# Kernel optimization log

Hardware: AMD Instinct MI355X
Metric: run time of the kernel (lower is better)

The kernel has to match this reference:

```python
import jax, jax.numpy as jnp
import numpy as np

KK = 10.0  # sigmoid sharpness constant `kk` from the source

def sigmoid_k(x):
    return jax.nn.sigmoid(KK * x)

def setup_inputs() -> dict:
    key = jax.random.key(0)
    k1, k2, k3 = jax.random.split(key, 3)
    B, L = 8192, 4096
    # contiguous valid-prefix padding mask with random per-row lengths in [L//4, L)
    lens = jax.random.randint(k1, (B,), L // 4, L)
    mask = (jnp.arange(L)[None, :] < lens[:, None]).astype(jnp.float32)
    t = jax.random.uniform(k2, (B, 1), dtype=jnp.float32) * L          # crop centers
    l = 1.0 + jax.random.uniform(k3, (B, 1), dtype=jnp.float32) * (L / 2.0)  # half-widths
    return {"t": t, "l": l, "mask": mask, "length": L}

def reference(t, l, mask, length):
    t = t.reshape(-1, 1)
    l = l.reshape(-1, 1)
    # boundaries of the valid region (replaces the CPU numpy argmax round-trip)
    left = (jnp.argmax(mask, axis=-1).astype(jnp.float32) - 1.0)[:, None]          # [B,1]
    right = (float(length) - jnp.argmax(mask[:, ::-1], axis=-1).astype(jnp.float32))[:, None]  # [B,1]
    sentence_length = jnp.sum(mask, axis=-1, keepdims=True) / 2.0                   # [B,1]
    l_eff = jnp.where(l <= sentence_length, sentence_length, l)
    t_left = (t - l_eff) * (t - l_eff >= left).astype(jnp.float32)
    t_left = jnp.where(t_left == 0.0, left, t_left)
    t_right = ((t + l_eff) <= right).astype(jnp.float32) * (t + l_eff)
    t_right = jnp.where(t_right == 0.0, right, t_right)
    pos = jnp.arange(length, dtype=jnp.float32)                                     # [L]
    crop_mask = sigmoid_k(pos - t_left) - sigmoid_k(pos - t_right)                  # [B,L]
    crop_mask = (crop_mask >= 0.5).astype(jnp.float32) * mask
    return crop_mask
```

## Files before the change

### kernel.cpp

```cpp
#include <hip/hip_runtime.h>
#include <hip/hip_bf16.h>
#include <climits>


#define BLOCK 256

typedef float nfloat4 __attribute__((ext_vector_type(4)));

__device__ __forceinline__ float sigmoid10(float x) {
    return 1.0f / (1.0f + expf(-10.0f * x));
}
__device__ __forceinline__ float fdiff(float p, float tl, float tr) {
    return sigmoid10(p - tl) - sigmoid10(p - tr);
}

__global__ __launch_bounds__(BLOCK) void probe_kernel(
    const float* __restrict__ t, const float* __restrict__ l,
    const float* __restrict__ mask, int2* __restrict__ ws, int B, int Llen) {
    const int row = blockIdx.x * BLOCK + threadIdx.x;
    if (row >= B) return;
    const float* mrow = mask + (size_t)row * Llen;

    int blo = -1, bhi = Llen;
    #pragma unroll 1
    for (int it = 0; it < 13; ++it) {
        int mid = (blo + bhi) >> 1;
        mid = max(mid, 0);
        const float v = mrow[mid];
        if (v > 0.5f) blo = mid; else bhi = mid;
    }
    const int len = bhi;

    int lo = 1, hi = 0;
    if (len > 0) {
        const float leftf  = -1.0f;
        const float rightf = (float)len;
        const float sl = 0.5f * (float)len;
        const float tv = t[row], lv = l[row];
        const float leff = (lv <= sl) ? sl : lv;
        float tl0 = tv - leff;
        float t_left = (tl0 >= leftf) ? tl0 : 0.0f;
        if (t_left == 0.0f) t_left = leftf;
        float tr0 = tv + leff;
        float t_right = (tr0 <= rightf) ? tr0 : 0.0f;
        if (t_right == 0.0f) t_right = rightf;

        const float c = expf(-10.0f * (t_right - t_left));
        const float b = 1.0f - 3.0f * c;
        const float disc = b * b - 4.0f * c;
        if (b > 0.0f && disc >= 0.0f) {
            const float xp = 0.5f * (b + sqrtf(disc));
            const float p_lo = t_left - 0.1f * logf(xp);
            const float p_hi = (t_left + t_right) - p_lo;
            lo = (int)ceilf(p_lo);
            hi = (int)floorf(p_hi);
            #pragma unroll 1
            for (int k = 0; k < 4 && fdiff((float)(lo - 1), t_left, t_right) >= 0.5f; ++k) --lo;
            #pragma unroll 1
            for (int k = 0; k < 4 && fdiff((float)lo, t_left, t_right) < 0.5f; ++k) ++lo;
            #pragma unroll 1
            for (int k = 0; k < 4 && fdiff((float)(hi + 1), t_left, t_right) >= 0.5f; ++k) ++hi;
            #pragma unroll 1
            for (int k = 0; k < 4 && fdiff((float)hi, t_left, t_right) < 0.5f; ++k) --hi;
        }
        lo = max(lo, 0);
        hi = min(hi, len - 1);
    }
    ws[row] = make_int2(lo, hi);
}

__global__ __launch_bounds__(BLOCK) void ones_kernel(
    const int2* __restrict__ ws, nfloat4* __restrict__ out,
    int nv, int B, int total_waves) {
    const int lane = threadIdx.x & 63;
    const int wave0 = blockIdx.x * (BLOCK / 64) + (threadIdx.x >> 6);

    for (int row = wave0; row < B; row += total_waves) {
        const int2 bnd = ws[row];
        const int lo = bnd.x, hi = bnd.y;
        if (lo > hi) continue;
        const int qA = lo >> 2, qB = hi >> 2;
        nfloat4* orow = out + (size_t)row * nv;
        for (int q = qA + lane; q <= qB; q += 64) {
            const int e = q << 2;
            nfloat4 o;
            o.x = (e     >= lo && e     <= hi) ? 1.0f : 0.0f;
            o.y = (e + 1 >= lo && e + 1 <= hi) ? 1.0f : 0.0f;
            o.z = (e + 2 >= lo && e + 2 <= hi) ? 1.0f : 0.0f;
            o.w = (e + 3 >= lo && e + 3 <= hi) ? 1.0f : 0.0f;
            __builtin_nontemporal_store(o, &orow[q]);
        }
    }
}

extern "C" void kernel_launch(void* const* d_in, const int* in_sizes, int n_in,
                              void* d_out, int out_size, void* d_ws, size_t ws_size,
                              hipStream_t stream) {
    const float* t    = (const float*)d_in[0];
    const float* l    = (const float*)d_in[1];
    const float* mask = (const float*)d_in[2];
    float* out = (float*)d_out;
    int2* ws = (int2*)d_ws;

    const int B = in_sizes[0];
    const int Llen = in_sizes[2] / B;

    hipMemsetAsync(d_out, 0, (size_t)out_size * sizeof(float), stream);

    probe_kernel<<<(B + BLOCK - 1) / BLOCK, BLOCK, 0, stream>>>(t, l, mask, ws, B, Llen);

    const int nv = Llen >> 2;
    const int blocks = 2048;
    const int total_waves = blocks * (BLOCK / 64);
    ones_kernel<<<blocks, BLOCK, 0, stream>>>(ws, (nfloat4*)out, nv, B, total_waves);
}
```

Measured before the change: 224.3 us.

## Drop memset and write full output rows with streaming stores

Removes the separate memset of the output and has the emit kernel write every element of each row, zeros included, so the output is written once instead of memset followed by partial overwrite. Each block handles 32 rows, loading their bounds into shared memory, and stores use inline global_store_dwordx4 with sc0 sc1 nt cache bits. The cost is that each row is written in full by one kernel, plus inline asm that depends on the target ISA.

```diff
diff --git a/kernel.cpp b/kernel.cpp
--- a/kernel.cpp
+++ b/kernel.cpp
@@ -4,8 +4,14 @@
 
 
 #define BLOCK 256
+#define ROWS_PER_BLOCK 32
 
 typedef float nfloat4 __attribute__((ext_vector_type(4)));
+
+__device__ __forceinline__ void store_stream(nfloat4 v, nfloat4* p) {
+    asm volatile("global_store_dwordx4 %0, %1, off sc0 sc1 nt"
+                 :: "v"(p), "v"(v) : "memory");
+}
 
 __device__ __forceinline__ float sigmoid10(float x) {
     return 1.0f / (1.0f + expf(-10.0f * x));
@@ -69,26 +75,42 @@
     ws[row] = make_int2(lo, hi);
 }
 
-__global__ __launch_bounds__(BLOCK) void ones_kernel(
-    const int2* __restrict__ ws, nfloat4* __restrict__ out,
-    int nv, int B, int total_waves) {
-    const int lane = threadIdx.x & 63;
-    const int wave0 = blockIdx.x * (BLOCK / 64) + (threadIdx.x >> 6);
+__global__ __launch_bounds__(BLOCK) void emit_kernel(
+    const int2* __restrict__ ws, nfloat4* __restrict__ out, int nv, int B) {
+    const int tid = threadIdx.x;
+    const int row0 = blockIdx.x * ROWS_PER_BLOCK;
 
-    for (int row = wave0; row < B; row += total_waves) {
-        const int2 bnd = ws[row];
-        const int lo = bnd.x, hi = bnd.y;
-        if (lo > hi) continue;
-        const int qA = lo >> 2, qB = hi >> 2;
+    __shared__ int2 s_bnd[ROWS_PER_BLOCK];
+    if (tid < ROWS_PER_BLOCK && row0 + tid < B)
+        s_bnd[tid] = ws[row0 + tid];
+    __syncthreads();
+
+    const int qpt = nv / BLOCK;
+    for (int r = 0; r < ROWS_PER_BLOCK; ++r) {
+        const int row = row0 + r;
+        if (row >= B) break;
+        const int lo = s_bnd[r].x, hi = s_bnd[r].y;
         nfloat4* orow = out + (size_t)row * nv;
-        for (int q = qA + lane; q <= qB; q += 64) {
+        #pragma unroll
+        for (int k = 0; k < 4; ++k) {
+            if (k >= qpt) break;
+            const int q = tid + k * BLOCK;
             const int e = q << 2;
             nfloat4 o;
             o.x = (e     >= lo && e     <= hi) ? 1.0f : 0.0f;
             o.y = (e + 1 >= lo && e + 1 <= hi) ? 1.0f : 0.0f;
             o.z = (e + 2 >= lo && e + 2 <= hi) ? 1.0f : 0.0f;
             o.w = (e + 3 >= lo && e + 3 <= hi) ? 1.0f : 0.0f;
-            __builtin_nontemporal_store(o, &orow[q]);
+            store_stream(o, &orow[q]);
+        }
+        for (int q = 4 * BLOCK + tid; q < nv; q += BLOCK) {
+            const int e = q << 2;
+            nfloat4 o;
+            o.x = (e     >= lo && e     <= hi) ? 1.0f : 0.0f;
+            o.y = (e + 1 >= lo && e + 1 <= hi) ? 1.0f : 0.0f;
+            o.z = (e + 2 >= lo && e + 2 <= hi) ? 1.0f : 0.0f;
+            o.w = (e + 3 >= lo && e + 3 <= hi) ? 1.0f : 0.0f;
+            store_stream(o, &orow[q]);
         }
     }
 }
@@ -105,12 +127,9 @@
     const int B = in_sizes[0];
     const int Llen = in_sizes[2] / B;
 
-    hipMemsetAsync(d_out, 0, (size_t)out_size * sizeof(float), stream);
-
     probe_kernel<<<(B + BLOCK - 1) / BLOCK, BLOCK, 0, stream>>>(t, l, mask, ws, B, Llen);
 
     const int nv = Llen >> 2;
-    const int blocks = 2048;
-    const int total_waves = blocks * (BLOCK / 64);
-    ones_kernel<<<blocks, BLOCK, 0, stream>>>(ws, (nfloat4*)out, nv, B, total_waves);
+    const int blocks = (B + ROWS_PER_BLOCK - 1) / ROWS_PER_BLOCK;
+    emit_kernel<<<blocks, BLOCK, 0, stream>>>(ws, (nfloat4*)out, nv, B);
 }
```

After: 220.6 us. No clear change (-1.6%).
